# Kernel tuning notes

Measured on AMD Instinct MI355X. Metric: run time of the kernel, lower is better.

The kernel has to match this reference:

```python
import jax, jax.numpy as jnp
import numpy as np
from jax import lax

B, N, D = 4, 4096, 1024
H, DH, K = 8, 128, 256  # heads, dim_head, linformer k
KERNEL = 32
PAD = (15, 16)  # torch padding='same' for even kernel: left=(k-1)//2, right=rest


def setup_inputs() -> dict:
    key = jax.random.key(0)
    ks = jax.random.split(key, 7)
    s = 0.02
    return {
        "x": jax.random.normal(ks[0], (B, N, D), dtype=jnp.float32),
        "Wq": jax.random.normal(ks[1], (D, D), dtype=jnp.float32) * s,
        "Wk": jax.random.normal(ks[2], (D, D), dtype=jnp.float32) * s,
        "Wpk": jax.random.normal(ks[3], (K, N, KERNEL), dtype=jnp.float32) * s,
        "bpk": jax.random.normal(ks[4], (K,), dtype=jnp.float32) * s,
        "Wo": jax.random.normal(ks[5], (D, D), dtype=jnp.float32) * s,
        "bo": jax.random.normal(ks[6], (D,), dtype=jnp.float32) * s,
    }


def reference(x, Wq, Wk, Wpk, bpk, Wo, bo):
    b, n, d = x.shape
    # linear projections (torch Linear: y = x @ W.T)
    q = x @ Wq.T                       # (b, n, h*dh)
    keys = x @ Wk.T                    # (b, n, h*dh)
    # Conv1d over feature length with seq positions as channels: (b, n, d) -> (b, k, d)
    keys = lax.conv_general_dilated(
        keys, Wpk, window_strides=(1,), padding=[PAD],
        dimension_numbers=("NCH", "OIH", "NCH"),
    ) + bpk[None, :, None]             # (b, K, h*dh)
    values = keys                      # share_kv=True
    # split heads
    q = q.reshape(b, n, H, DH).transpose(0, 2, 1, 3)        # (b, h, n, dh)
    kk = keys.reshape(b, K, H, DH).transpose(0, 2, 1, 3)    # (b, h, K, dh)
    vv = values.reshape(b, K, H, DH).transpose(0, 2, 1, 3)  # (b, h, K, dh)
    dots = jnp.einsum("bhnd,bhkd->bhnk", q, kk) * (DH ** -0.5)
    attn = jax.nn.softmax(dots, axis=-1)                    # dropout p=0.0 (eval)
    out = jnp.einsum("bhnk,bhkd->bhnd", attn, vv)
    out = out.transpose(0, 2, 1, 3).reshape(b, n, H * DH)
    return out @ Wo.T + bo
```

## Files before the change

kernel.cpp:

```cpp
#include <hip/hip_runtime.h>


typedef short v8s __attribute__((ext_vector_type(8)));
typedef float v4f __attribute__((ext_vector_type(4)));

#define MFMA16(a, b, c) __builtin_amdgcn_mfma_f32_16x16x32_bf16((a), (b), (c), 0, 0, 0)

__device__ __forceinline__ unsigned short f2bf(float f) {
  unsigned int u = __float_as_uint(f);
  u += 0x7fffu + ((u >> 16) & 1u);
  return (unsigned short)(u >> 16);
}

__device__ __forceinline__ v8s cvt8(float4 a, float4 b) {
  v8s v;
  v[0] = (short)f2bf(a.x); v[1] = (short)f2bf(a.y);
  v[2] = (short)f2bf(a.z); v[3] = (short)f2bf(a.w);
  v[4] = (short)f2bf(b.x); v[5] = (short)f2bf(b.y);
  v[6] = (short)f2bf(b.z); v[7] = (short)f2bf(b.w);
  return v;
}

__device__ __forceinline__ void gld16(void* lds, const void* g) {
  __builtin_amdgcn_global_load_lds(
      (const __attribute__((address_space(1))) void*)g,
      (__attribute__((address_space(3))) void*)lds, 16, 0, 0);
}

__device__ __forceinline__ const v8s* frag_ptr(const short* base, int row, int g) {
  return (const v8s*)(base + row * 32 + (((g ^ (row >> 1)) & 3) << 3));
}

__global__ __launch_bounds__(256) void k_cvt(const float* __restrict__ src,
                                             short* __restrict__ dst, int n8) {
  const int i = blockIdx.x * 256 + threadIdx.x;
  if (i >= n8) return;
  const float4* s = (const float4*)src;
  ((v8s*)dst)[i] = cvt8(s[2 * i], s[2 * i + 1]);
}

__global__ __launch_bounds__(256) void k_reorder_wpk(const float* __restrict__ Wpk,
                                                     short* __restrict__ Wr) {
  __shared__ short T[64][40];
  const int k  = blockIdx.x >> 6;
  const int n0 = (blockIdx.x & 63) << 6;
  const int tid = threadIdx.x;
  {
    const int i = tid >> 2, t0 = (tid & 3) << 3;
    const float* p = Wpk + ((size_t)k * 4096 + n0 + i) * 32 + t0;
    float4 a = *(const float4*)p, b = *(const float4*)(p + 4);
    *(v8s*)&T[i][t0] = cvt8(a, b);
  }
  __syncthreads();
  {
    const int t = tid >> 3, j0 = (tid & 7) << 3;
    v8s o;
#pragma unroll
    for (int q = 0; q < 8; ++q) o[q] = T[j0 + q][t];
    *(v8s*)(Wr + ((size_t)t * 256 + k) * 4096 + n0 + j0) = o;
  }
}

__global__ __launch_bounds__(256) void k_init_kc(const float* __restrict__ bpk,
                                                 float* __restrict__ Kc) {
  const int idx = (blockIdx.x * 256 + threadIdx.x) * 4;
  const float v = bpk[(idx >> 10) & 255];
  float4 f; f.x = v; f.y = v; f.z = v; f.w = v;
  *(float4*)(Kc + idx) = f;
}

__global__ __launch_bounds__(256) void k_zero_pad(short* __restrict__ KpTp) {
  const int idx = blockIdx.x * 256 + threadIdx.x;
  const int ridx = idx >> 9, col8 = idx & 511;
  const int b = ridx >> 5, rr = ridx & 31;
  const int row = (rr < 15) ? rr : 1039 + (rr - 15);
  v8s z = {0, 0, 0, 0, 0, 0, 0, 0};
  *(v8s*)(KpTp + ((size_t)b * 1056 + row) * 4096 + col8 * 8) = z;
}

__global__ __launch_bounds__(256) void k_gemm_qk_v2(const short* __restrict__ xbf,
                                                    const short* __restrict__ Wqk,
                                                    short* __restrict__ Qbf,
                                                    short* __restrict__ Kp) {
  __shared__ short As[2][128][32];
  __shared__ short Bs[2][128][32];
  const int tid = threadIdx.x, lane = tid & 63, w = tid >> 6;
  const int m0 = blockIdx.x * 128, j0 = blockIdx.y * 128;
  const int wr = (w >> 1) * 64, wc = (w & 1) * 64;
  const int l15 = lane & 15, g = lane >> 4;
  const int sr = lane >> 2, sseg = lane & 3;

  v4f acc[4][4];
#pragma unroll
  for (int i = 0; i < 4; ++i)
#pragma unroll
    for (int j = 0; j < 4; ++j) acc[i][j] = (v4f)0.0f;

  auto stage = [&](int buf, int k0) {
#pragma unroll
    for (int q0 = 0; q0 < 2; ++q0) {
      const int rblk = (w * 2 + q0) << 4, r = rblk + sr;
      const int co = ((sseg ^ (r >> 1)) & 3) << 3;
      gld16(&As[buf][rblk][0], xbf + (size_t)(m0 + r) * 1024 + k0 + co);
      gld16(&Bs[buf][rblk][0], Wqk + (size_t)(j0 + r) * 1024 + k0 + co);
    }
  };

  stage(0, 0);
  __syncthreads();
#pragma unroll 1
  for (int k0 = 0, buf = 0; k0 < 1024; k0 += 32, buf ^= 1) {
    if (k0 + 32 < 1024) stage(buf ^ 1, k0 + 32);
    v8s af[4], bf4[4];
#pragma unroll
    for (int mi = 0; mi < 4; ++mi)
      af[mi] = *frag_ptr(&As[buf][0][0], wr + mi * 16 + l15, g);
#pragma unroll
    for (int ni = 0; ni < 4; ++ni)
      bf4[ni] = *frag_ptr(&Bs[buf][0][0], wc + ni * 16 + l15, g);
#pragma unroll
    for (int ni = 0; ni < 4; ++ni)
#pragma unroll
      for (int mi = 0; mi < 4; ++mi)
        acc[mi][ni] = MFMA16(af[mi], bf4[ni], acc[mi][ni]);
    __syncthreads();
  }
  const int rbase = (lane >> 4) * 4;
#pragma unroll
  for (int mi = 0; mi < 4; ++mi)
#pragma unroll
    for (int ni = 0; ni < 4; ++ni) {
      const int col = j0 + wc + ni * 16 + l15;
      short* dst = (col < 1024) ? Qbf : Kp;
      const int cj = (col < 1024) ? col : col - 1024;
#pragma unroll
      for (int r = 0; r < 4; ++r) {
        const int row = m0 + wr + mi * 16 + rbase + r;
        dst[(size_t)row * 1024 + cj] = (short)f2bf(acc[mi][ni][r]);
      }
    }
}

__global__ __launch_bounds__(256) void k_transpose_pad(const short* __restrict__ src,
                                                       short* __restrict__ dst) {
  __shared__ short T[64][72];
  const int r0 = blockIdx.x * 64, c0 = blockIdx.y * 64, b = blockIdx.z;
  const int tid = threadIdx.x;
  {
    const int i = tid >> 2, q = (tid & 3) << 4;
    const short* ps = src + ((size_t)b * 4096 + r0 + i) * 1024 + c0 + q;
    *(v8s*)&T[i][q]     = *(const v8s*)ps;
    *(v8s*)&T[i][q + 8] = *(const v8s*)(ps + 8);
  }
  __syncthreads();
  {
    const int j = tid >> 2, p = (tid & 3) << 4;
    v8s o0, o1;
#pragma unroll
    for (int t = 0; t < 8; ++t) o0[t] = T[p + t][j];
#pragma unroll
    for (int t = 0; t < 8; ++t) o1[t] = T[p + 8 + t][j];
    short* pd = dst + ((size_t)b * 1056 + 15 + c0 + j) * 4096 + r0 + p;
    *(v8s*)pd = o0;
    *(v8s*)(pd + 8) = o1;
  }
}

__global__ __launch_bounds__(256) void k_conv_v2(const short* __restrict__ Wr,
                                                 const short* __restrict__ KpTp,
                                                 float* __restrict__ Kc) {
  __shared__ short As[2][2][128][32];
  __shared__ short Kt[2][160][32];
  const int L = blockIdx.x;
  const int xcd = L & 7, jj = L >> 3;
  const int slice = xcd + ((jj >> 5) << 3), win = jj & 31;
  const int mt = slice >> 3, ns = slice & 7, nt = win >> 2, b = win & 3;
  const int K0 = mt * 128, D0 = nt * 128;
  const int tid = threadIdx.x, lane = tid & 63, w = tid >> 6;
  const int wr = (w >> 1) * 64, wc = (w & 1) * 64;
  const int l15 = lane & 15, g = lane >> 4;
  const int sr = lane >> 2, sseg = lane & 3;
  const short* KpTb = KpTp + (size_t)b * 1056 * 4096;

  v4f acc[4][4];
#pragma unroll
  for (int i = 0; i < 4; ++i)
#pragma unroll
    for (int j = 0; j < 4; ++j) acc[i][j] = (v4f)0.0f;

  auto stageAs = [&](int buf, int nc, int tp) {
    const int n0 = ns * 512 + nc * 32, t0 = tp * 2;
#pragma unroll
    for (int q0 = 0; q0 < 4; ++q0) {
      const int q = w + q0 * 4;
      const int pl = q >> 3, rblk = (q & 7) << 4, r = rblk + sr;
      gld16(&As[buf][pl][rblk][0],
            Wr + ((size_t)(t0 + pl) * 256 + K0 + r) * 4096 + n0 +
                (((sseg ^ (r >> 1)) & 3) << 3));
    }
  };
  auto stageKt = [&](int buf, int nc) {
    const int n0 = ns * 512 + nc * 32;
    for (int q = w; q < 10; q += 4) {
      const int rblk = q << 4, r = rblk + sr;
      gld16(&Kt[buf][rblk][0],
            KpTb + (size_t)(D0 + r) * 4096 + n0 + (((sseg ^ (r >> 1)) & 3) << 3));
    }
  };

  stageKt(0, 0);
  stageAs(0, 0, 0);
  __syncthreads();
  int ab = 0, kb = 0;
#pragma unroll 1
  for (int ph = 0; ph < 256; ++ph) {
    const int tp = ph & 15;
    if (ph < 255) {
      const int nn = (ph + 1) >> 4, np = (ph + 1) & 15;
      stageAs(ab ^ 1, nn, np);
      if (np == 0) stageKt(kb ^ 1, nn);
    }
#pragma unroll
    for (int pl = 0; pl < 2; ++pl) {
      const int t = tp * 2 + pl;
      v8s af[4], bf4[4];
#pragma unroll
      for (int mi = 0; mi < 4; ++mi)
        af[mi] = *frag_ptr(&As[ab][pl][0][0], wr + mi * 16 + l15, g);
#pragma unroll
      for (int ni = 0; ni < 4; ++ni)
        bf4[ni] = *frag_ptr(&Kt[kb][0][0], wc + ni * 16 + l15 + t, g);
#pragma unroll
      for (int ni = 0; ni < 4; ++ni)
#pragma unroll
        for (int mi = 0; mi < 4; ++mi)
          acc[mi][ni] = MFMA16(af[mi], bf4[ni], acc[mi][ni]);
    }
    __syncthreads();
    ab ^= 1;
    kb ^= (tp == 15) ? 1 : 0;
  }

  float* kcb = Kc + (size_t)b * 256 * 1024;
  const int rbase = (lane >> 4) * 4;
#pragma unroll
  for (int mi = 0; mi < 4; ++mi)
#pragma unroll
    for (int ni = 0; ni < 4; ++ni)
#pragma unroll
      for (int r = 0; r < 4; ++r)
        atomicAdd(kcb + (size_t)(K0 + wr + mi * 16 + rbase + r) * 1024 +
                      (D0 + wc + ni * 16 + l15),
                  acc[mi][ni][r]);
}

__global__ __launch_bounds__(256) void k_kc_post(const float* __restrict__ Kc,
                                                 short* __restrict__ Kcbf,
                                                 short* __restrict__ KcT) {
  __shared__ short T[64][72];
  const int k0 = blockIdx.x * 64, d0 = blockIdx.y * 64, b = blockIdx.z;
  const int tid = threadIdx.x;
  {
    const int i = tid >> 2, q = (tid & 3) << 4;
    const float* ps = Kc + (size_t)(b * 256 + k0 + i) * 1024 + d0 + q;
    float4 f0 = *(const float4*)ps,       f1 = *(const float4*)(ps + 4);
    float4 f2 = *(const float4*)(ps + 8), f3 = *(const float4*)(ps + 12);
    v8s v0 = cvt8(f0, f1), v1 = cvt8(f2, f3);
    *(v8s*)&T[i][q] = v0;
    *(v8s*)&T[i][q + 8] = v1;
    short* pc = Kcbf + (size_t)(b * 256 + k0 + i) * 1024 + d0 + q;
    *(v8s*)pc = v0;
    *(v8s*)(pc + 8) = v1;
  }
  __syncthreads();
  {
    const int j = tid >> 2, p = (tid & 3) << 4;
    v8s o0, o1;
#pragma unroll
    for (int t = 0; t < 8; ++t) o0[t] = T[p + t][j];
#pragma unroll
    for (int t = 0; t < 8; ++t) o1[t] = T[p + 8 + t][j];
    short* pd = KcT + (size_t)(b * 1024 + d0 + j) * 256 + k0 + p;
    *(v8s*)pd = o0;
    *(v8s*)(pd + 8) = o1;
  }
}

__global__ __launch_bounds__(256) void k_attn(const short* __restrict__ Qbf,
                                              const short* __restrict__ Kcbf,
                                              const short* __restrict__ KcT,
                                              short* __restrict__ AO) {
  __shared__ short P[4][16][264];
  const int nt = blockIdx.x, h = blockIdx.y, b = blockIdx.z;
  const int tid = threadIdx.x, lane = tid & 63, w = tid >> 6;
  const int l15 = lane & 15, lg4 = (lane >> 4) * 4, lg8 = (lane >> 4) * 8;
  const float scale = 0.08838834764831845f;
  const size_t qb  = (size_t)b * 4096 * 1024 + (size_t)h * 128;
  const size_t kb  = (size_t)b * 256 * 1024 + (size_t)h * 128;
  const size_t vtb = ((size_t)b * 1024 + (size_t)h * 128) * 256;
  short (*Pw)[264] = P[w];
  const int n_wave = nt * 128 + w * 32;

#pragma unroll 1
  for (int half = 0; half < 2; ++half) {
    const int nbase = n_wave + half * 16;
    v8s aq[4];
#pragma unroll
    for (int kt = 0; kt < 4; ++kt)
      aq[kt] = *(const v8s*)(Qbf + qb + (size_t)(nbase + l15) * 1024 + kt * 32 + lg8);

    v4f dacc[16];
#pragma unroll
    for (int ct = 0; ct < 16; ++ct) dacc[ct] = (v4f)0.0f;
#pragma unroll 1
    for (int kt = 0; kt < 4; ++kt) {
#pragma unroll
      for (int ct = 0; ct < 16; ++ct) {
        v8s bk = *(const v8s*)(Kcbf + kb + (size_t)(ct * 16 + l15) * 1024 + kt * 32 + lg8);
        dacc[ct] = MFMA16(aq[kt], bk, dacc[ct]);
      }
    }
#pragma unroll
    for (int ct = 0; ct < 16; ++ct) dacc[ct] = dacc[ct] * scale;
    v4f m4 = dacc[0];
#pragma unroll
    for (int ct = 1; ct < 16; ++ct)
#pragma unroll
      for (int r = 0; r < 4; ++r) m4[r] = fmaxf(m4[r], dacc[ct][r]);
#pragma unroll
    for (int off = 1; off < 16; off <<= 1)
#pragma unroll
      for (int r = 0; r < 4; ++r) m4[r] = fmaxf(m4[r], __shfl_xor(m4[r], off, 64));
    v4f ssum = (v4f)0.0f;
#pragma unroll
    for (int ct = 0; ct < 16; ++ct)
#pragma unroll
      for (int r = 0; r < 4; ++r) {
        const float e = __expf(dacc[ct][r] - m4[r]);
        ssum[r] += e;
        Pw[lg4 + r][ct * 16 + l15] = (short)f2bf(e);
      }
#pragma unroll
    for (int off = 1; off < 16; off <<= 1)
#pragma unroll
      for (int r = 0; r < 4; ++r) ssum[r] += __shfl_xor(ssum[r], off, 64);
    __syncthreads();

    v4f oacc[8];
#pragma unroll
    for (int ct = 0; ct < 8; ++ct) oacc[ct] = (v4f)0.0f;
#pragma unroll 1
    for (int kt2 = 0; kt2 < 8; ++kt2) {
      v8s pa = *(const v8s*)&Pw[l15][kt2 * 32 + lg8];
#pragma unroll
      for (int ct = 0; ct < 8; ++ct) {
        v8s bv = *(const v8s*)(KcT + vtb + (size_t)(ct * 16 + l15) * 256 + kt2 * 32 + lg8);
        oacc[ct] = MFMA16(pa, bv, oacc[ct]);
      }
    }
    v4f inv;
#pragma unroll
    for (int r = 0; r < 4; ++r) inv[r] = 1.0f / ssum[r];
#pragma unroll
    for (int ct = 0; ct < 8; ++ct)
#pragma unroll
      for (int r = 0; r < 4; ++r)
        AO[qb + (size_t)(nbase + lg4 + r) * 1024 + ct * 16 + l15] =
            (short)f2bf(oacc[ct][r] * inv[r]);
    __syncthreads();
  }
}

__global__ __launch_bounds__(256) void k_gemm_out_v2(const short* __restrict__ AO,
                                                     const short* __restrict__ Wobf,
                                                     const float* __restrict__ bo,
                                                     float* __restrict__ out) {
  __shared__ short As[2][128][32];
  __shared__ short Bs[2][128][32];
  const int tid = threadIdx.x, lane = tid & 63, w = tid >> 6;
  const int m0 = blockIdx.x * 128, j0 = blockIdx.y * 128;
  const int wr = (w >> 1) * 64, wc = (w & 1) * 64;
  const int l15 = lane & 15, g = lane >> 4;
  const int sr = lane >> 2, sseg = lane & 3;

  v4f acc[4][4];
#pragma unroll
  for (int i = 0; i < 4; ++i)
#pragma unroll
    for (int j = 0; j < 4; ++j) acc[i][j] = (v4f)0.0f;

  auto stage = [&](int buf, int k0) {
#pragma unroll
    for (int q0 = 0; q0 < 2; ++q0) {
      const int rblk = (w * 2 + q0) << 4, r = rblk + sr;
      const int co = ((sseg ^ (r >> 1)) & 3) << 3;
      gld16(&As[buf][rblk][0], AO + (size_t)(m0 + r) * 1024 + k0 + co);
      gld16(&Bs[buf][rblk][0], Wobf + (size_t)(j0 + r) * 1024 + k0 + co);
    }
  };

  stage(0, 0);
  __syncthreads();
#pragma unroll 1
  for (int k0 = 0, buf = 0; k0 < 1024; k0 += 32, buf ^= 1) {
    if (k0 + 32 < 1024) stage(buf ^ 1, k0 + 32);
    v8s af[4], bf4[4];
#pragma unroll
    for (int mi = 0; mi < 4; ++mi)
      af[mi] = *frag_ptr(&As[buf][0][0], wr + mi * 16 + l15, g);
#pragma unroll
    for (int ni = 0; ni < 4; ++ni)
      bf4[ni] = *frag_ptr(&Bs[buf][0][0], wc + ni * 16 + l15, g);
#pragma unroll
    for (int ni = 0; ni < 4; ++ni)
#pragma unroll
      for (int mi = 0; mi < 4; ++mi)
        acc[mi][ni] = MFMA16(af[mi], bf4[ni], acc[mi][ni]);
    __syncthreads();
  }
  const int rbase = (lane >> 4) * 4;
#pragma unroll
  for (int mi = 0; mi < 4; ++mi)
#pragma unroll
    for (int ni = 0; ni < 4; ++ni) {
      const int col = j0 + wc + ni * 16 + l15;
      const float bias = bo[col];
#pragma unroll
      for (int r = 0; r < 4; ++r) {
        const int row = m0 + wr + mi * 16 + rbase + r;
        out[(size_t)row * 1024 + col] = acc[mi][ni][r] + bias;
      }
    }
}

extern "C" void kernel_launch(void* const* d_in, const int* in_sizes, int n_in,
                              void* d_out, int out_size, void* d_ws, size_t ws_size,
                              hipStream_t stream) {
  const float* x   = (const float*)d_in[0];
  const float* Wq  = (const float*)d_in[1];
  const float* Wk  = (const float*)d_in[2];
  const float* Wpk = (const float*)d_in[3];
  const float* bpk = (const float*)d_in[4];
  const float* Wo  = (const float*)d_in[5];
  const float* bo  = (const float*)d_in[6];

  const size_t OFF_WR   = 0;
  const size_t OFF_XBF  = 67108864;
  const size_t OFF_WQK  = 100663296;
  const size_t OFF_KPTP = 67108864;
  const size_t OFF_KCBF = 67108864;
  const size_t OFF_KCT  = 69206016;
  const size_t OFF_WOBF = 101711872;
  const size_t OFF_QBF  = 104857600;
  const size_t OFF_KP   = 138412032;
  const size_t OFF_KC   = 171966464;
  const size_t NEED     = 176160768;
  if (ws_size < NEED) return;

  char* ws = (char*)d_ws;
  short* Wr   = (short*)(ws + OFF_WR);
  short* xbf  = (short*)(ws + OFF_XBF);
  short* Wqk  = (short*)(ws + OFF_WQK);
  short* KpTp = (short*)(ws + OFF_KPTP);
  short* Kcbf = (short*)(ws + OFF_KCBF);
  short* KcT  = (short*)(ws + OFF_KCT);
  short* Wobf = (short*)(ws + OFF_WOBF);
  short* Qbf  = (short*)(ws + OFF_QBF);
  short* Kp   = (short*)(ws + OFF_KP);
  float* Kc   = (float*)(ws + OFF_KC);
  short* AO   = Kp;
  float* outp = (float*)d_out;

  k_cvt<<<dim3(8192), dim3(256), 0, stream>>>(x, xbf, 16777216 / 8);
  k_cvt<<<dim3(512),  dim3(256), 0, stream>>>(Wq, Wqk, 1048576 / 8);
  k_cvt<<<dim3(512),  dim3(256), 0, stream>>>(Wk, Wqk + 1048576, 1048576 / 8);
  k_reorder_wpk<<<dim3(16384), dim3(256), 0, stream>>>(Wpk, Wr);
  k_init_kc<<<dim3(1024), dim3(256), 0, stream>>>(bpk, Kc);
  k_gemm_qk_v2<<<dim3(128, 16), dim3(256), 0, stream>>>(xbf, Wqk, Qbf, Kp);
  k_transpose_pad<<<dim3(64, 16, 4), dim3(256), 0, stream>>>(Kp, KpTp);
  k_cvt<<<dim3(512), dim3(256), 0, stream>>>(Wo, Wobf, 1048576 / 8);
  k_zero_pad<<<dim3(256), dim3(256), 0, stream>>>(KpTp);
  k_conv_v2<<<dim3(512), dim3(256), 0, stream>>>(Wr, KpTp, Kc);
  k_kc_post<<<dim3(4, 16, 4), dim3(256), 0, stream>>>(Kc, Kcbf, KcT);
  k_attn<<<dim3(32, 8, 4), dim3(256), 0, stream>>>(Qbf, Kcbf, KcT, AO);
  k_gemm_out_v2<<<dim3(128, 8), dim3(256), 0, stream>>>(AO, Wobf, bo, outp);
}
```

Baseline: 643.9 us.

## Use explicit vmcnt waits and triple-buffer conv staging for deeper prefetch

The GEMM and conv main loops replace __syncthreads, which waits for every outstanding global load, with partial s_waitcnt vmcnt waits plus raw barriers. This lets the next stage's global-to-LDS loads stay in flight while the current tile is computed. The conv kernel also moves to a three-deep LDS ring for the weight tiles, prefetching two phases ahead and issuing the Kt tile earlier. The cost is more LDS for the conv kernel and hand-counted vmcnt values, which break if the number of loads issued per stage ever changes.

```diff
diff --git a/kernel.cpp b/kernel.cpp
--- a/kernel.cpp
+++ b/kernel.cpp
@@ -5,6 +5,8 @@
 typedef float v4f __attribute__((ext_vector_type(4)));
 
 #define MFMA16(a, b, c) __builtin_amdgcn_mfma_f32_16x16x32_bf16((a), (b), (c), 0, 0, 0)
+#define WAITV(N) asm volatile("s_waitcnt vmcnt(" #N ")" ::: "memory")
+#define SBAR() __builtin_amdgcn_s_barrier()
 
 __device__ __forceinline__ unsigned short f2bf(float f) {
   unsigned int u = __float_as_uint(f);
@@ -78,7 +80,7 @@
   *(v8s*)(KpTp + ((size_t)b * 1056 + row) * 4096 + col8 * 8) = z;
 }
 
-__global__ __launch_bounds__(256) void k_gemm_qk_v2(const short* __restrict__ xbf,
+__global__ __launch_bounds__(256) void k_gemm_qk_v3(const short* __restrict__ xbf,
                                                     const short* __restrict__ Wqk,
                                                     short* __restrict__ Qbf,
                                                     short* __restrict__ Kp) {
@@ -107,10 +109,11 @@
   };
 
   stage(0, 0);
-  __syncthreads();
-#pragma unroll 1
-  for (int k0 = 0, buf = 0; k0 < 1024; k0 += 32, buf ^= 1) {
-    if (k0 + 32 < 1024) stage(buf ^ 1, k0 + 32);
+#pragma unroll 1
+  for (int p = 0, buf = 0; p < 32; ++p, buf ^= 1) {
+    if (p + 1 < 32) stage(buf ^ 1, (p + 1) * 32);
+    if (p < 31) { WAITV(4); } else { WAITV(0); }
+    SBAR();
     v8s af[4], bf4[4];
 #pragma unroll
     for (int mi = 0; mi < 4; ++mi)
@@ -123,7 +126,7 @@
 #pragma unroll
       for (int mi = 0; mi < 4; ++mi)
         acc[mi][ni] = MFMA16(af[mi], bf4[ni], acc[mi][ni]);
-    __syncthreads();
+    SBAR();
   }
   const int rbase = (lane >> 4) * 4;
 #pragma unroll
@@ -166,10 +169,10 @@
   }
 }
 
-__global__ __launch_bounds__(256) void k_conv_v2(const short* __restrict__ Wr,
+__global__ __launch_bounds__(256) void k_conv_v3(const short* __restrict__ Wr,
                                                  const short* __restrict__ KpTp,
                                                  float* __restrict__ Kc) {
-  __shared__ short As[2][2][128][32];
+  __shared__ short As[3][2][128][32];
   __shared__ short Kt[2][160][32];
   const int L = blockIdx.x;
   const int xcd = L & 7, jj = L >> 3;
@@ -188,8 +191,8 @@
 #pragma unroll
     for (int j = 0; j < 4; ++j) acc[i][j] = (v4f)0.0f;
 
-  auto stageAs = [&](int buf, int nc, int tp) {
-    const int n0 = ns * 512 + nc * 32, t0 = tp * 2;
+  auto stageAs = [&](int buf, int ph) {
+    const int n0 = ns * 512 + (ph >> 4) * 32, t0 = (ph & 15) * 2;
 #pragma unroll
     for (int q0 = 0; q0 < 4; ++q0) {
       const int q = w + q0 * 4;
@@ -209,24 +212,26 @@
   };
 
   stageKt(0, 0);
-  stageAs(0, 0, 0);
-  __syncthreads();
-  int ab = 0, kb = 0;
-#pragma unroll 1
-  for (int ph = 0; ph < 256; ++ph) {
-    const int tp = ph & 15;
-    if (ph < 255) {
-      const int nn = (ph + 1) >> 4, np = (ph + 1) & 15;
-      stageAs(ab ^ 1, nn, np);
-      if (np == 0) stageKt(kb ^ 1, nn);
-    }
+  stageAs(0, 0);
+  stageAs(1, 1);
+  int kb = 0;
+#pragma unroll 1
+  for (int p = 0; p < 256; ++p) {
+    const int tp = p & 15;
+    if (p + 2 < 256) {
+      stageAs((p + 2) % 3, p + 2);
+      if (tp == 14) stageKt(kb ^ 1, (p + 2) >> 4);
+    }
+    if (p < 254) { WAITV(8); } else if (p == 254) { WAITV(4); } else { WAITV(0); }
+    SBAR();
+    const short* Ab = &As[p % 3][0][0][0];
 #pragma unroll
     for (int pl = 0; pl < 2; ++pl) {
       const int t = tp * 2 + pl;
       v8s af[4], bf4[4];
 #pragma unroll
       for (int mi = 0; mi < 4; ++mi)
-        af[mi] = *frag_ptr(&As[ab][pl][0][0], wr + mi * 16 + l15, g);
+        af[mi] = *frag_ptr(Ab + pl * 128 * 32, wr + mi * 16 + l15, g);
 #pragma unroll
       for (int ni = 0; ni < 4; ++ni)
         bf4[ni] = *frag_ptr(&Kt[kb][0][0], wc + ni * 16 + l15 + t, g);
@@ -236,9 +241,8 @@
         for (int mi = 0; mi < 4; ++mi)
           acc[mi][ni] = MFMA16(af[mi], bf4[ni], acc[mi][ni]);
     }
-    __syncthreads();
-    ab ^= 1;
-    kb ^= (tp == 15) ? 1 : 0;
+    SBAR();
+    if (tp == 15) kb ^= 1;
   }
 
   float* kcb = Kc + (size_t)b * 256 * 1024;
@@ -371,7 +375,7 @@
   }
 }
 
-__global__ __launch_bounds__(256) void k_gemm_out_v2(const short* __restrict__ AO,
+__global__ __launch_bounds__(256) void k_gemm_out_v3(const short* __restrict__ AO,
                                                      const short* __restrict__ Wobf,
                                                      const float* __restrict__ bo,
                                                      float* __restrict__ out) {
@@ -400,10 +404,11 @@
   };
 
   stage(0, 0);
-  __syncthreads();
-#pragma unroll 1
-  for (int k0 = 0, buf = 0; k0 < 1024; k0 += 32, buf ^= 1) {
-    if (k0 + 32 < 1024) stage(buf ^ 1, k0 + 32);
+#pragma unroll 1
+  for (int p = 0, buf = 0; p < 32; ++p, buf ^= 1) {
+    if (p + 1 < 32) stage(buf ^ 1, (p + 1) * 32);
+    if (p < 31) { WAITV(4); } else { WAITV(0); }
+    SBAR();
     v8s af[4], bf4[4];
 #pragma unroll
     for (int mi = 0; mi < 4; ++mi)
@@ -416,7 +421,7 @@
 #pragma unroll
       for (int mi = 0; mi < 4; ++mi)
         acc[mi][ni] = MFMA16(af[mi], bf4[ni], acc[mi][ni]);
-    __syncthreads();
+    SBAR();
   }
   const int rbase = (lane >> 4) * 4;
 #pragma unroll
@@ -476,12 +481,12 @@
   k_cvt<<<dim3(512),  dim3(256), 0, stream>>>(Wk, Wqk + 1048576, 1048576 / 8);
   k_reorder_wpk<<<dim3(16384), dim3(256), 0, stream>>>(Wpk, Wr);
   k_init_kc<<<dim3(1024), dim3(256), 0, stream>>>(bpk, Kc);
-  k_gemm_qk_v2<<<dim3(128, 16), dim3(256), 0, stream>>>(xbf, Wqk, Qbf, Kp);
+  k_gemm_qk_v3<<<dim3(128, 16), dim3(256), 0, stream>>>(xbf, Wqk, Qbf, Kp);
   k_transpose_pad<<<dim3(64, 16, 4), dim3(256), 0, stream>>>(Kp, KpTp);
   k_cvt<<<dim3(512), dim3(256), 0, stream>>>(Wo, Wobf, 1048576 / 8);
   k_zero_pad<<<dim3(256), dim3(256), 0, stream>>>(KpTp);
-  k_conv_v2<<<dim3(512), dim3(256), 0, stream>>>(Wr, KpTp, Kc);
+  k_conv_v3<<<dim3(512), dim3(256), 0, stream>>>(Wr, KpTp, Kc);
   k_kc_post<<<dim3(4, 16, 4), dim3(256), 0, stream>>>(Kc, Kcbf, KcT);
   k_attn<<<dim3(32, 8, 4), dim3(256), 0, stream>>>(Qbf, Kcbf, KcT, AO);
-  k_gemm_out_v2<<<dim3(128, 8), dim3(256), 0, stream>>>(AO, Wobf, bo, outp);
-}
+  k_gemm_out_v3<<<dim3(128, 8), dim3(256), 0, stream>>>(AO, Wobf, bo, outp);
+}
```

New measurement: 638.4 us. Within noise of the previous version (-0.9%).
